# Kernel tuning notes

Hardware: AMD Instinct MI355X
Metric: run time of the kernel (lower is better)

Reference implementation:

```python
import jax, jax.numpy as jnp
import numpy as np

X_DIM, Y_DIM, HIDDEN, N = 768, 768, 300, 768


def setup_inputs() -> dict:
    key = jax.random.key(0)
    ks = jax.random.split(key, 7)
    lim1 = 1.0 / np.sqrt(X_DIM + Y_DIM)
    lim2 = 1.0 / np.sqrt(HIDDEN)
    return {
        "x_samples": jax.random.normal(ks[0], (N, X_DIM), dtype=jnp.float32),
        "y_samples": jax.random.normal(ks[1], (N, Y_DIM), dtype=jnp.float32),
        "perm": jax.random.permutation(ks[2], N).astype(jnp.int32),
        # Linear 1: (x_dim+y_dim) -> hidden, torch default uniform init
        "W1": jax.random.uniform(ks[3], (HIDDEN, X_DIM + Y_DIM), jnp.float32, -lim1, lim1),
        "b1": jax.random.uniform(ks[4], (HIDDEN,), jnp.float32, -lim1, lim1),
        # Linear 2: hidden -> 1
        "W2": jax.random.uniform(ks[5], (1, HIDDEN), jnp.float32, -lim2, lim2),
        "b2": jax.random.uniform(ks[6], (1,), jnp.float32, -lim2, lim2),
    }


def reference(x_samples, y_samples, perm, W1, b1, W2, b2):
    n = x_samples.shape[0]
    x_dim = x_samples.shape[1]
    # First linear is separable across the concat: split W1 into x- and y-parts.
    hx = x_samples @ W1[:, :x_dim].T            # [N, H]
    hy = y_samples @ W1[:, x_dim:].T            # [N, H]
    w2 = W2[0]                                   # [H]
    # T0: matched pairs (x_i, y_i)
    t0 = jax.nn.softplus(jax.nn.relu(hx + hy + b1) @ w2 + b2[0])   # [N]
    # T1[i, j] = F(x_j, y_perm[i]) -- pairwise tile, [N, N, H] intermediate
    hyp = hy[perm]                               # [N, H]
    hpair = jax.nn.relu(hyp[:, None, :] + hx[None, :, :] + b1)     # [N, N, H]
    t1 = jax.nn.softplus(hpair @ w2 + b2[0])     # [N, N]
    lower_bound = t0.mean() - (jax.nn.logsumexp(t1, axis=1).mean() - jnp.log(n).astype(t1.dtype))
    return lower_bound
```

## Files before the change

kernel.cpp:

```cpp
#include <hip/hip_runtime.h>
#include <math.h>

#define NN   768
#define HH   300
#define HP   320
#define KD   768

#define P_OFF    0
#define PKS_STR  245760
#define PG_STR   1966080
#define CF_OFF   3932160
#define AF_OFF   4177920
#define RS_OFF   4423680
#define T0_OFF   4435968

__global__ __launch_bounds__(256) void k1_gemm(
    const float* __restrict__ x, const float* __restrict__ y,
    const int* __restrict__ perm, const float* __restrict__ W1,
    float* __restrict__ wsf)
{
    const int tid = threadIdx.x;
    const int tx = tid & 15;
    const int ty = tid >> 4;
    const int i0 = blockIdx.x * 128;
    const int h0 = blockIdx.y * 64;
    const int g  = blockIdx.z & 1;
    const int ks = blockIdx.z >> 1;
    const int kbeg = ks * 96;

    const float* src = g ? y : x;
    const int koff = g ? KD : 0;

    __shared__ float Xt[32][132];
    __shared__ float Wt[32][68];

    float acc[4][8];
    #pragma unroll
    for (int r = 0; r < 4; ++r)
        #pragma unroll
        for (int cc = 0; cc < 8; ++cc) acc[r][cc] = 0.f;

    const int kq = (tid & 7) << 2;
    const float* xp[4];
    int xr[4];
    #pragma unroll
    for (int it = 0; it < 4; ++it) {
        int row = ((tid + it*256) >> 3);
        int gr = i0 + row;
        if (g) gr = perm[gr];
        xp[it] = src + (size_t)gr * KD + kbeg + kq;
        xr[it] = row;
    }
    const float* wp[2];
    int wr[2]; bool wv[2];
    #pragma unroll
    for (int it = 0; it < 2; ++it) {
        int hrow = ((tid + it*256) >> 3);
        int hg = h0 + hrow;
        wv[it] = hg < HH;
        wp[it] = W1 + (size_t)(wv[it] ? hg : 0) * (2*KD) + koff + kbeg + kq;
        wr[it] = hrow;
    }

    for (int kb = 0; kb < 96; kb += 32) {
        float4 xv[4], wvv[2];
        #pragma unroll
        for (int it = 0; it < 4; ++it) xv[it] = *(const float4*)(xp[it] + kb);
        #pragma unroll
        for (int it = 0; it < 2; ++it) {
            wvv[it] = *(const float4*)(wp[it] + kb);
            if (!wv[it]) wvv[it] = make_float4(0,0,0,0);
        }
        if (kb) __syncthreads();
        #pragma unroll
        for (int it = 0; it < 4; ++it) {
            Xt[kq+0][xr[it]] = xv[it].x; Xt[kq+1][xr[it]] = xv[it].y;
            Xt[kq+2][xr[it]] = xv[it].z; Xt[kq+3][xr[it]] = xv[it].w;
        }
        #pragma unroll
        for (int it = 0; it < 2; ++it) {
            Wt[kq+0][wr[it]] = wvv[it].x; Wt[kq+1][wr[it]] = wvv[it].y;
            Wt[kq+2][wr[it]] = wvv[it].z; Wt[kq+3][wr[it]] = wvv[it].w;
        }
        __syncthreads();

        #pragma unroll 8
        for (int k = 0; k < 32; ++k) {
            float4 a  = *(const float4*)&Wt[k][4*ty];
            float4 b0 = *(const float4*)&Xt[k][4*tx];
            float4 b1v = *(const float4*)&Xt[k][64 + 4*tx];
            float ar[4] = {a.x, a.y, a.z, a.w};
            float br[8] = {b0.x, b0.y, b0.z, b0.w, b1v.x, b1v.y, b1v.z, b1v.w};
            #pragma unroll
            for (int r = 0; r < 4; ++r)
                #pragma unroll
                for (int cc = 0; cc < 8; ++cc)
                    acc[r][cc] = fmaf(ar[r], br[cc], acc[r][cc]);
        }
    }

    float* dst = wsf + P_OFF + (size_t)(g*8 + ks) * PKS_STR;
    #pragma unroll
    for (int cc = 0; cc < 8; ++cc) {
        int i = i0 + ((cc >> 2) ? 64 : 0) + 4*tx + (cc & 3);
        float4 v = make_float4(acc[0][cc], acc[1][cc], acc[2][cc], acc[3][cc]);
        *(float4*)(dst + (size_t)i * HP + h0 + 4*ty) = v;
    }
}

__global__ __launch_bounds__(256) void k1b_combine(
    const float* __restrict__ b1, float* __restrict__ wsf)
{
    int idx = blockIdx.x * 256 + threadIdx.x;
    int g = idx >= 61440;
    int rem = idx - g * 61440;
    int i = rem / 80;
    int h4 = (rem % 80) * 4;

    float4 o = make_float4(0.f,0.f,0.f,0.f);
    const float* p = wsf + P_OFF + (size_t)g * PG_STR + (size_t)i * HP + h4;
    #pragma unroll
    for (int ks = 0; ks < 8; ++ks) {
        float4 v = *(const float4*)(p + (size_t)ks * PKS_STR);
        o.x += v.x; o.y += v.y; o.z += v.z; o.w += v.w;
    }
    if (g && h4 < HH) {
        float4 bv = *(const float4*)(b1 + h4);
        o.x += bv.x; o.y += bv.y; o.z += bv.z; o.w += bv.w;
    }
    float* dst = wsf + (g ? AF_OFF : CF_OFF) + (size_t)i * HP + h4;
    *(float4*)dst = o;
}

__global__ __launch_bounds__(256) void k2_pair(
    const float* __restrict__ wsf, const float* __restrict__ w2,
    const int* __restrict__ perm, const float* __restrict__ b2,
    float* __restrict__ rsO, float* __restrict__ t0c)
{
    const int tid = threadIdx.x;
    const int tx = tid & 15;
    const int ty = tid >> 4;
    const int j0 = blockIdx.x * 48;
    const int i0 = blockIdx.y * 48;

    const float* AF = wsf + AF_OFF;
    const float* CF = wsf + CF_OFF;

    __shared__ __align__(16) float As[48][156];
    __shared__ __align__(16) float Cs[48][156];
    __shared__ __align__(16) float w2s[304];

    if (tid < 76) {
        float4 wv = make_float4(0.f,0.f,0.f,0.f);
        if (tid < 75) wv = *(const float4*)(w2 + 4*tid);
        *(float4*)&w2s[4*tid] = wv;
    }

    float acc[3][3];
    #pragma unroll
    for (int r = 0; r < 3; ++r)
        #pragma unroll
        for (int c = 0; c < 3; ++c) acc[r][c] = 0.f;

    #pragma unroll
    for (int ch = 0; ch < 2; ++ch) {
        const int hbeg = ch * 152;
        const int nq = ch ? 37 : 38;
        if (ch) __syncthreads();
        for (int e = tid; e < 48 * nq; e += 256) {
            int i = e / nq, q = e % nq;
            *(float4*)&As[i][4*q] =
                *(const float4*)(AF + (size_t)(i0 + i) * HP + hbeg + 4*q);
            *(float4*)&Cs[i][4*q] =
                *(const float4*)(CF + (size_t)(j0 + i) * HP + hbeg + 4*q);
        }
        __syncthreads();

        #pragma unroll 2
        for (int k = 0; k < nq; ++k) {
            float4 wq = *(const float4*)&w2s[hbeg + 4*k];
            float4 a0 = *(const float4*)&As[ty     ][4*k];
            float4 a1 = *(const float4*)&As[ty + 16][4*k];
            float4 a2 = *(const float4*)&As[ty + 32][4*k];
            float4 c0 = *(const float4*)&Cs[tx     ][4*k];
            float4 c1 = *(const float4*)&Cs[tx + 16][4*k];
            float4 c2 = *(const float4*)&Cs[tx + 32][4*k];
            const float* wp = (const float*)&wq;
            const float* ap0 = (const float*)&a0;
            const float* ap1 = (const float*)&a1;
            const float* ap2 = (const float*)&a2;
            const float* cp0 = (const float*)&c0;
            const float* cp1 = (const float*)&c1;
            const float* cp2 = (const float*)&c2;
            #pragma unroll
            for (int hh = 0; hh < 4; ++hh) {
                float wh = wp[hh];
                float av0 = ap0[hh], av1 = ap1[hh], av2 = ap2[hh];
                float cv0 = cp0[hh], cv1 = cp1[hh], cv2 = cp2[hh];
                acc[0][0] = fmaf(fmaxf(av0 + cv0, 0.f), wh, acc[0][0]);
                acc[0][1] = fmaf(fmaxf(av0 + cv1, 0.f), wh, acc[0][1]);
                acc[0][2] = fmaf(fmaxf(av0 + cv2, 0.f), wh, acc[0][2]);
                acc[1][0] = fmaf(fmaxf(av1 + cv0, 0.f), wh, acc[1][0]);
                acc[1][1] = fmaf(fmaxf(av1 + cv1, 0.f), wh, acc[1][1]);
                acc[1][2] = fmaf(fmaxf(av1 + cv2, 0.f), wh, acc[1][2]);
                acc[2][0] = fmaf(fmaxf(av2 + cv0, 0.f), wh, acc[2][0]);
                acc[2][1] = fmaf(fmaxf(av2 + cv1, 0.f), wh, acc[2][1]);
                acc[2][2] = fmaf(fmaxf(av2 + cv2, 0.f), wh, acc[2][2]);
            }
        }
    }

    const float b2v = b2[0];
    #pragma unroll
    for (int r = 0; r < 3; ++r) {
        int i = i0 + ty + 16 * r;
        int pj = perm[i];
        float rsum = 0.f;
        #pragma unroll
        for (int c = 0; c < 3; ++c) {
            int j = j0 + tx + 16 * c;
            float u = acc[r][c] + b2v;
            rsum += expf(u);
            if (j == pj)
                t0c[i] = (u > 0.f) ? u + log1pf(expf(-u)) : log1pf(expf(u));
        }
        #pragma unroll
        for (int off = 8; off; off >>= 1)
            rsum += __shfl_xor(rsum, off, 16);
        if (tx == 0) rsO[(size_t)blockIdx.x * NN + i] = rsum;
    }
}

__global__ __launch_bounds__(256) void k3_final(
    const float* __restrict__ wsf, float* __restrict__ out)
{
    const int tid = threadIdx.x;
    const float* rs = wsf + RS_OFF;
    const float* t0 = wsf + T0_OFF;

    double st0 = 0.0, slse = 0.0;
    for (int i = tid; i < NN; i += 256) {
        float s = 0.f;
        #pragma unroll
        for (int jb = 0; jb < 16; ++jb) s += rs[(size_t)jb * NN + i];
        st0  += (double)t0[i];
        slse += log((double)NN + (double)s);
    }
    __shared__ double sa[256], sb[256];
    sa[tid] = st0; sb[tid] = slse;
    __syncthreads();
    for (int s = 128; s > 0; s >>= 1) {
        if (tid < s) { sa[tid] += sa[tid+s]; sb[tid] += sb[tid+s]; }
        __syncthreads();
    }
    if (tid == 0) {
        double lb = sa[0]/(double)NN - (sb[0]/(double)NN - log((double)NN));
        out[0] = (float)lb;
    }
}

extern "C" void kernel_launch(void* const* d_in, const int* in_sizes, int n_in,
                              void* d_out, int out_size, void* d_ws, size_t ws_size,
                              hipStream_t stream) {
    const float* x    = (const float*)d_in[0];
    const float* y    = (const float*)d_in[1];
    const int*   perm = (const int*)  d_in[2];
    const float* W1   = (const float*)d_in[3];
    const float* b1   = (const float*)d_in[4];
    const float* W2   = (const float*)d_in[5];
    const float* b2   = (const float*)d_in[6];
    float* wsf = (float*)d_ws;
    float* out = (float*)d_out;

    k1_gemm    <<<dim3(6,5,16), 256, 0, stream>>>(x, y, perm, W1, wsf);
    k1b_combine<<<480,          256, 0, stream>>>(b1, wsf);
    k2_pair    <<<dim3(16,16),  256, 0, stream>>>(wsf, W2, perm, b2,
                                                  wsf + RS_OFF, wsf + T0_OFF);
    k3_final   <<<1,            256, 0, stream>>>(wsf, out);
}
```

Measured before the change: 117.4 us.

## Split pairwise hidden reduction across two thread halves and halve GEMM k-splits

The pairwise kernel now runs 512 threads per block, with each half computing the relu-weighted sum over one half of the hidden dimension in parallel. Partial sums are combined through shared memory before the softplus/exp epilogue, and the sequential two-chunk loop with its extra barrier is removed. Separately, the first GEMM uses 4 k-splits of 192 instead of 8 of 96, so fewer partial buffers are written and summed. This doubles the shared memory per block and gives the GEMM fewer, longer blocks, which may lower occupancy.

```diff
diff --git a/kernel.cpp b/kernel.cpp
--- a/kernel.cpp
+++ b/kernel.cpp
@@ -8,11 +8,11 @@
 
 #define P_OFF    0
 #define PKS_STR  245760
-#define PG_STR   1966080
-#define CF_OFF   3932160
-#define AF_OFF   4177920
-#define RS_OFF   4423680
-#define T0_OFF   4435968
+#define PG_STR   983040
+#define CF_OFF   1966080
+#define AF_OFF   2211840
+#define RS_OFF   2457600
+#define T0_OFF   2469888
 
 __global__ __launch_bounds__(256) void k1_gemm(
     const float* __restrict__ x, const float* __restrict__ y,
@@ -26,7 +26,7 @@
     const int h0 = blockIdx.y * 64;
     const int g  = blockIdx.z & 1;
     const int ks = blockIdx.z >> 1;
-    const int kbeg = ks * 96;
+    const int kbeg = ks * 192;
 
     const float* src = g ? y : x;
     const int koff = g ? KD : 0;
@@ -62,7 +62,7 @@
         wr[it] = hrow;
     }
 
-    for (int kb = 0; kb < 96; kb += 32) {
+    for (int kb = 0; kb < 192; kb += 32) {
         float4 xv[4], wvv[2];
         #pragma unroll
         for (int it = 0; it < 4; ++it) xv[it] = *(const float4*)(xp[it] + kb);
@@ -86,8 +86,8 @@
 
         #pragma unroll 8
         for (int k = 0; k < 32; ++k) {
-            float4 a  = *(const float4*)&Wt[k][4*ty];
-            float4 b0 = *(const float4*)&Xt[k][4*tx];
+            float4 a   = *(const float4*)&Wt[k][4*ty];
+            float4 b0  = *(const float4*)&Xt[k][4*tx];
             float4 b1v = *(const float4*)&Xt[k][64 + 4*tx];
             float ar[4] = {a.x, a.y, a.z, a.w};
             float br[8] = {b0.x, b0.y, b0.z, b0.w, b1v.x, b1v.y, b1v.z, b1v.w};
@@ -99,7 +99,7 @@
         }
     }
 
-    float* dst = wsf + P_OFF + (size_t)(g*8 + ks) * PKS_STR;
+    float* dst = wsf + P_OFF + (size_t)(g*4 + ks) * PKS_STR;
     #pragma unroll
     for (int cc = 0; cc < 8; ++cc) {
         int i = i0 + ((cc >> 2) ? 64 : 0) + 4*tx + (cc & 3);
@@ -120,7 +120,7 @@
     float4 o = make_float4(0.f,0.f,0.f,0.f);
     const float* p = wsf + P_OFF + (size_t)g * PG_STR + (size_t)i * HP + h4;
     #pragma unroll
-    for (int ks = 0; ks < 8; ++ks) {
+    for (int ks = 0; ks < 4; ++ks) {
         float4 v = *(const float4*)(p + (size_t)ks * PKS_STR);
         o.x += v.x; o.y += v.y; o.z += v.z; o.w += v.w;
     }
@@ -132,22 +132,25 @@
     *(float4*)dst = o;
 }
 
-__global__ __launch_bounds__(256) void k2_pair(
+__global__ __launch_bounds__(512, 2) void k2_pair(
     const float* __restrict__ wsf, const float* __restrict__ w2,
     const int* __restrict__ perm, const float* __restrict__ b2,
     float* __restrict__ rsO, float* __restrict__ t0c)
 {
-    const int tid = threadIdx.x;
-    const int tx = tid & 15;
-    const int ty = tid >> 4;
+    const int tid  = threadIdx.x;
+    const int half = tid >> 8;
+    const int t2   = tid & 255;
+    const int tx = t2 & 15;
+    const int ty = t2 >> 4;
     const int j0 = blockIdx.x * 48;
     const int i0 = blockIdx.y * 48;
+    const int hbeg = half * 152;
 
     const float* AF = wsf + AF_OFF;
     const float* CF = wsf + CF_OFF;
 
-    __shared__ __align__(16) float As[48][156];
-    __shared__ __align__(16) float Cs[48][156];
+    __shared__ __align__(16) float As[2][48][156];
+    __shared__ __align__(16) float Cs[2][48][156];
     __shared__ __align__(16) float w2s[304];
 
     if (tid < 76) {
@@ -155,6 +158,14 @@
         if (tid < 75) wv = *(const float4*)(w2 + 4*tid);
         *(float4*)&w2s[4*tid] = wv;
     }
+    for (int e = t2; e < 48 * 38; e += 256) {
+        int i = e / 38, q = e % 38;
+        *(float4*)&As[half][i][4*q] =
+            *(const float4*)(AF + (size_t)(i0 + i) * HP + hbeg + 4*q);
+        *(float4*)&Cs[half][i][4*q] =
+            *(const float4*)(CF + (size_t)(j0 + i) * HP + hbeg + 4*q);
+    }
+    __syncthreads();
 
     float acc[3][3];
     #pragma unroll
@@ -162,72 +173,71 @@
         #pragma unroll
         for (int c = 0; c < 3; ++c) acc[r][c] = 0.f;
 
-    #pragma unroll
-    for (int ch = 0; ch < 2; ++ch) {
-        const int hbeg = ch * 152;
-        const int nq = ch ? 37 : 38;
-        if (ch) __syncthreads();
-        for (int e = tid; e < 48 * nq; e += 256) {
-            int i = e / nq, q = e % nq;
-            *(float4*)&As[i][4*q] =
-                *(const float4*)(AF + (size_t)(i0 + i) * HP + hbeg + 4*q);
-            *(float4*)&Cs[i][4*q] =
-                *(const float4*)(CF + (size_t)(j0 + i) * HP + hbeg + 4*q);
-        }
-        __syncthreads();
-
-        #pragma unroll 2
-        for (int k = 0; k < nq; ++k) {
-            float4 wq = *(const float4*)&w2s[hbeg + 4*k];
-            float4 a0 = *(const float4*)&As[ty     ][4*k];
-            float4 a1 = *(const float4*)&As[ty + 16][4*k];
-            float4 a2 = *(const float4*)&As[ty + 32][4*k];
-            float4 c0 = *(const float4*)&Cs[tx     ][4*k];
-            float4 c1 = *(const float4*)&Cs[tx + 16][4*k];
-            float4 c2 = *(const float4*)&Cs[tx + 32][4*k];
-            const float* wp = (const float*)&wq;
-            const float* ap0 = (const float*)&a0;
-            const float* ap1 = (const float*)&a1;
-            const float* ap2 = (const float*)&a2;
-            const float* cp0 = (const float*)&c0;
-            const float* cp1 = (const float*)&c1;
-            const float* cp2 = (const float*)&c2;
-            #pragma unroll
-            for (int hh = 0; hh < 4; ++hh) {
-                float wh = wp[hh];
-                float av0 = ap0[hh], av1 = ap1[hh], av2 = ap2[hh];
-                float cv0 = cp0[hh], cv1 = cp1[hh], cv2 = cp2[hh];
-                acc[0][0] = fmaf(fmaxf(av0 + cv0, 0.f), wh, acc[0][0]);
-                acc[0][1] = fmaf(fmaxf(av0 + cv1, 0.f), wh, acc[0][1]);
-                acc[0][2] = fmaf(fmaxf(av0 + cv2, 0.f), wh, acc[0][2]);
-                acc[1][0] = fmaf(fmaxf(av1 + cv0, 0.f), wh, acc[1][0]);
-                acc[1][1] = fmaf(fmaxf(av1 + cv1, 0.f), wh, acc[1][1]);
-                acc[1][2] = fmaf(fmaxf(av1 + cv2, 0.f), wh, acc[1][2]);
-                acc[2][0] = fmaf(fmaxf(av2 + cv0, 0.f), wh, acc[2][0]);
-                acc[2][1] = fmaf(fmaxf(av2 + cv1, 0.f), wh, acc[2][1]);
-                acc[2][2] = fmaf(fmaxf(av2 + cv2, 0.f), wh, acc[2][2]);
+    #pragma unroll 2
+    for (int k = 0; k < 38; ++k) {
+        float4 wq = *(const float4*)&w2s[hbeg + 4*k];
+        float4 a0 = *(const float4*)&As[half][ty     ][4*k];
+        float4 a1 = *(const float4*)&As[half][ty + 16][4*k];
+        float4 a2 = *(const float4*)&As[half][ty + 32][4*k];
+        float4 c0 = *(const float4*)&Cs[half][tx     ][4*k];
+        float4 c1 = *(const float4*)&Cs[half][tx + 16][4*k];
+        float4 c2 = *(const float4*)&Cs[half][tx + 32][4*k];
+        const float* wp  = (const float*)&wq;
+        const float* ap0 = (const float*)&a0;
+        const float* ap1 = (const float*)&a1;
+        const float* ap2 = (const float*)&a2;
+        const float* cp0 = (const float*)&c0;
+        const float* cp1 = (const float*)&c1;
+        const float* cp2 = (const float*)&c2;
+        #pragma unroll
+        for (int hh = 0; hh < 4; ++hh) {
+            float wh = wp[hh];
+            float av0 = ap0[hh], av1 = ap1[hh], av2 = ap2[hh];
+            float cv0 = cp0[hh], cv1 = cp1[hh], cv2 = cp2[hh];
+            acc[0][0] = fmaf(fmaxf(av0 + cv0, 0.f), wh, acc[0][0]);
+            acc[0][1] = fmaf(fmaxf(av0 + cv1, 0.f), wh, acc[0][1]);
+            acc[0][2] = fmaf(fmaxf(av0 + cv2, 0.f), wh, acc[0][2]);
+            acc[1][0] = fmaf(fmaxf(av1 + cv0, 0.f), wh, acc[1][0]);
+            acc[1][1] = fmaf(fmaxf(av1 + cv1, 0.f), wh, acc[1][1]);
+            acc[1][2] = fmaf(fmaxf(av1 + cv2, 0.f), wh, acc[1][2]);
+            acc[2][0] = fmaf(fmaxf(av2 + cv0, 0.f), wh, acc[2][0]);
+            acc[2][1] = fmaf(fmaxf(av2 + cv1, 0.f), wh, acc[2][1]);
+            acc[2][2] = fmaf(fmaxf(av2 + cv2, 0.f), wh, acc[2][2]);
+        }
+    }
+
+    __syncthreads();
+    float* comb = &As[0][0][0];
+    if (half) {
+        float* cp = comb + t2 * 9;
+        #pragma unroll
+        for (int r = 0; r < 3; ++r)
+            #pragma unroll
+            for (int c = 0; c < 3; ++c) cp[r*3 + c] = acc[r][c];
+    }
+    __syncthreads();
+
+    if (half == 0) {
+        const float* cp = comb + t2 * 9;
+        const float b2v = b2[0];
+        #pragma unroll
+        for (int r = 0; r < 3; ++r) {
+            int i = i0 + ty + 16 * r;
+            int pj = perm[i];
+            float rsum = 0.f;
+            #pragma unroll
+            for (int c = 0; c < 3; ++c) {
+                int j = j0 + tx + 16 * c;
+                float u = acc[r][c] + cp[r*3 + c] + b2v;
+                rsum += expf(u);
+                if (j == pj)
+                    t0c[i] = (u > 0.f) ? u + log1pf(expf(-u)) : log1pf(expf(u));
             }
-        }
-    }
-
-    const float b2v = b2[0];
-    #pragma unroll
-    for (int r = 0; r < 3; ++r) {
-        int i = i0 + ty + 16 * r;
-        int pj = perm[i];
-        float rsum = 0.f;
-        #pragma unroll
-        for (int c = 0; c < 3; ++c) {
-            int j = j0 + tx + 16 * c;
-            float u = acc[r][c] + b2v;
-            rsum += expf(u);
-            if (j == pj)
-                t0c[i] = (u > 0.f) ? u + log1pf(expf(-u)) : log1pf(expf(u));
-        }
-        #pragma unroll
-        for (int off = 8; off; off >>= 1)
-            rsum += __shfl_xor(rsum, off, 16);
-        if (tx == 0) rsO[(size_t)blockIdx.x * NN + i] = rsum;
+            #pragma unroll
+            for (int off = 8; off; off >>= 1)
+                rsum += __shfl_xor(rsum, off, 16);
+            if (tx == 0) rsO[(size_t)blockIdx.x * NN + i] = rsum;
+        }
     }
 }
 
@@ -272,9 +282,9 @@
     float* wsf = (float*)d_ws;
     float* out = (float*)d_out;
 
-    k1_gemm    <<<dim3(6,5,16), 256, 0, stream>>>(x, y, perm, W1, wsf);
+    k1_gemm    <<<dim3(6,5,8),  256, 0, stream>>>(x, y, perm, W1, wsf);
     k1b_combine<<<480,          256, 0, stream>>>(b1, wsf);
-    k2_pair    <<<dim3(16,16),  256, 0, stream>>>(wsf, W2, perm, b2,
+    k2_pair    <<<dim3(16,16),  512, 0, stream>>>(wsf, W2, perm, b2,
                                                   wsf + RS_OFF, wsf + T0_OFF);
     k3_final   <<<1,            256, 0, stream>>>(wsf, out);
 }
```

After: 115.5 us. No clear change (-1.6%).
